# Kernel optimization log

Measured on AMD Instinct MI355X. Metric: run time of the kernel, lower is better.

The kernel has to match this reference:

```python
import jax, jax.numpy as jnp
import numpy as np

EPS = 1e-5
CLIP = 1.0

@jax.custom_vjp
def ste_sign(x):
    return jnp.sign(x)

def _ste_fwd(x):
    return jnp.sign(x), x

def _ste_bwd(x, g):
    return (g * (jnp.abs(x) <= CLIP).astype(g.dtype),)

ste_sign.defvjp(_ste_fwd, _ste_bwd)

def conv2d(x, w, stride, pad):
    return jax.lax.conv_general_dilated(
        x, w, window_strides=(stride, stride), padding=[(pad, pad), (pad, pad)],
        dimension_numbers=('NCHW', 'OIHW', 'NCHW'))

def bn(x, g, b, m, v):
    inv = g / jnp.sqrt(v + EPS)
    return x * inv[None, :, None, None] + (b - m * inv)[None, :, None, None]

def setup_inputs() -> dict:
    key = jax.random.key(0)
    ks = jax.random.split(key, 16)
    def rn(k, shape, scale=0.05):
        return jax.random.normal(k, shape, dtype=jnp.float32) * scale
    C = [64, 128, 128, 192, 192]
    d = {}
    d['x'] = jax.random.normal(ks[0], (128, 1, 128, 128), dtype=jnp.float32)
    d['conv1_w'] = rn(ks[1], (C[0], 1, 3, 3), 0.3)
    d['conv1_b'] = rn(ks[2], (C[0],))
    d['w2'] = rn(ks[3], (C[1], C[0], 3, 3), 0.3)
    d['w3'] = rn(ks[4], (C[2], C[1], 3, 3), 0.3)
    d['w4'] = rn(ks[5], (C[3], C[2], 3, 3), 0.3)
    d['w5'] = rn(ks[6], (C[4], C[3], 1, 1), 0.3)
    d['conv6_w'] = rn(ks[7], (12, C[4], 1, 1), 0.1)
    d['conv6_b'] = rn(ks[8], (12,))
    d['fc_w'] = rn(ks[9], (12, 12), 0.2)
    d['fc_b'] = rn(ks[10], (12,))
    for i, c in enumerate(C):
        kk = jax.random.split(jax.random.fold_in(key, 100 + i), 4)
        d[f'bn{i+1}_g'] = 1.0 + rn(kk[0], (c,), 0.1)
        d[f'bn{i+1}_b'] = rn(kk[1], (c,), 0.1)
        d[f'bn{i+1}_m'] = rn(kk[2], (c,), 0.1)
        d[f'bn{i+1}_v'] = 1.0 + jnp.abs(rn(kk[3], (c,), 0.1))
    return d

def reference(x, conv1_w, conv1_b, w2, w3, w4, w5, conv6_w, conv6_b, fc_w, fc_b,
              bn1_g, bn1_b, bn1_m, bn1_v, bn2_g, bn2_b, bn2_m, bn2_v,
              bn3_g, bn3_b, bn3_m, bn3_v, bn4_g, bn4_b, bn4_m, bn4_v,
              bn5_g, bn5_b, bn5_m, bn5_v):
    # conv1 (float) + BN + ReLU
    h = conv2d(x, conv1_w, 2, 1) + conv1_b[None, :, None, None]
    h = jax.nn.relu(bn(h, bn1_g, bn1_b, bn1_m, bn1_v))
    # binarized conv blocks: sign(activation) conv sign(weight)
    h = conv2d(ste_sign(h), ste_sign(w2), 1, 1)
    h = jax.nn.relu(bn(h, bn2_g, bn2_b, bn2_m, bn2_v))
    h = conv2d(ste_sign(h), ste_sign(w3), 2, 1)
    h = jax.nn.relu(bn(h, bn3_g, bn3_b, bn3_m, bn3_v))
    h = conv2d(ste_sign(h), ste_sign(w4), 1, 1)
    h = jax.nn.relu(bn(h, bn4_g, bn4_b, bn4_m, bn4_v))
    h = conv2d(ste_sign(h), ste_sign(w5), 1, 0)
    h = jax.nn.relu(bn(h, bn5_g, bn5_b, bn5_m, bn5_v))
    # 1x1 conv to classes, global average pool, FC, softmax
    h = conv2d(h, conv6_w, 1, 0) + conv6_b[None, :, None, None]
    h = jnp.mean(h, axis=(2, 3))  # [B, num_classes]
    logits = h @ fc_w.T + fc_b
    return jax.nn.softmax(logits, axis=1)
```

## Files before the change

kernel.cpp:

```cpp
#include <hip/hip_runtime.h>
#include <cstdint>

using u64 = unsigned long long;
using u32 = unsigned int;
typedef __attribute__((ext_vector_type(4))) int int4v;
typedef __attribute__((ext_vector_type(16))) int int16v;

struct PrepArgs {
  const float* bng[5]; const float* bnb[5]; const float* bnm[5]; const float* bnv[5];
  float* inv1; float* cc1; float* inv5; float* cc5;
  int* thr[3]; int* flp[3];
  const float* w[4];
  u64* wp[4]; u64* wz[4];
  u32* flags;
  const float* x; float* xpad;
  signed char* bf2x; signed char* bf3; signed char* bf4;
};

__device__ __forceinline__ void prep_all_body(const PrepArgs& a, int i) {
  if (i < 704) {
    const int off[6] = {0, 64, 192, 320, 512, 704};
    int l = 0;
    while (i >= off[l + 1]) ++l;
    int c = i - off[l];
    float iv = __fdiv_rn(a.bng[l][c], __fsqrt_rn(__fadd_rn(a.bnv[l][c], 1e-5f)));
    float cb = __fsub_rn(a.bnb[l][c], __fmul_rn(a.bnm[l][c], iv));
    if (l == 0) { a.inv1[c] = iv; a.cc1[c] = cb; }
    else if (l == 4) { a.inv5[c] = iv; a.cc5[c] = cb; }
    else {
      auto pred = [&](int v_) {
        return __fadd_rn(__fmul_rn((float)v_, iv), cb) > 0.f;
      };
      int Tx, fl;
      if (iv == 0.f) { Tx = pred(0) ? -100000 : 100000; fl = 0; }
      else if (iv > 0.f) {
        if (pred(-2048)) { Tx = -100000; fl = 0; }
        else if (!pred(2048)) { Tx = 100000; fl = 0; }
        else {
          int lo = -2048, hi = 2048;
          while (hi - lo > 1) { int md = (lo + hi) >> 1; if (pred(md)) hi = md; else lo = md; }
          Tx = hi; fl = 0;
        }
      } else {
        if (pred(2048)) { Tx = -100000; fl = -1; }
        else if (!pred(-2048)) { Tx = 100000; fl = -1; }
        else {
          int lo = -2048, hi = 2048;
          while (hi - lo > 1) { int md = (lo + hi) >> 1; if (pred(md)) lo = md; else hi = md; }
          Tx = lo ^ -1; fl = -1;
        }
      }
      a.thr[l - 1][c] = Tx; a.flp[l - 1][c] = fl;
    }
    return;
  }
  int j = i - 704;
  if (j >= 7488) return;
  const int poff[5] = {0, 1152, 3456, 6912, 7488};
  const int ICt[4] = {64, 128, 128, 192};
  const int Kt[4]  = {9, 9, 9, 1};
  const int Wt[4]  = {1, 2, 2, 3};
  int l = 0;
  while (j >= poff[l + 1]) ++l;
  int idx = j - poff[l];
  int W = Wt[l], K = Kt[l], IC = ICt[l];
  int wi = idx % W;
  int rest = idx / W;
  int t = rest % K;
  int oc = rest / K;
  u64 p = 0, z = 0;
  int icbase = wi * 64;
  int nb = IC - icbase; if (nb > 64) nb = 64;
  const float* w = a.w[l];
  for (int b = 0; b < nb; ++b) {
    float f = w[((size_t)oc * IC + (icbase + b)) * K + t];
    if (f > 0.f) p |= (1ull << b);
    else if (f == 0.f) z |= (1ull << b);
  }
  a.wp[l][idx] = p;
  a.wz[l][idx] = z;
  if (z) atomicOr(a.flags + l, 1u);
}

__device__ __forceinline__ void prep_bfrag32_body(const float* __restrict__ w,
                                                  signed char* __restrict__ bf, int idx) {
  if (idx >= 4 * 18 * 64) return;
  int lane = idx & 63;
  int rest = idx >> 6;
  int s = rest % 18;
  int t = rest / 18;
  int oc = t * 32 + (lane & 31);
  int kbase = s * 32 + (lane >> 5) * 16;
  signed char* dst = bf + (size_t)idx * 16;
#pragma unroll
  for (int i = 0; i < 16; ++i) {
    int k = kbase + i;
    int ch = k & 63, tap = k >> 6;
    float f = w[((size_t)oc * 64 + ch) * 9 + tap];
    dst[i] = (f > 0.f) ? 1 : ((f < 0.f) ? -1 : 0);
  }
}

template <int COUT>
__device__ __forceinline__ void prep_bfrag32b_body(const float* __restrict__ w,
                                                   signed char* __restrict__ bf, int idx) {
  constexpr int NT = COUT / 32;
  if (idx >= NT * 36 * 64) return;
  int lane = idx & 63;
  int rest = idx >> 6;
  int s = rest % 36;
  int t = rest / 36;
  int oc = t * 32 + (lane & 31);
  int kbase = s * 32 + (lane >> 5) * 16;
  signed char* dst = bf + (size_t)idx * 16;
#pragma unroll
  for (int i = 0; i < 16; ++i) {
    int k = kbase + i;
    int ch = k % 128, tap = k / 128;
    float f = w[((size_t)oc * 128 + ch) * 9 + tap];
    dst[i] = (f > 0.f) ? 1 : ((f < 0.f) ? -1 : 0);
  }
}

__global__ __launch_bounds__(256) void front(PrepArgs a) {
  int b = blockIdx.x, tid = threadIdx.x;
  if (b < 8192) {
    int idx = b * 256 + tid;
    int c = idx & 127, r = (idx >> 7) & 127, n = idx >> 14;
    a.xpad[((size_t)n * 130 + r + 1) * 136 + c + 1] = a.x[idx];
    return;
  }
  b -= 8192;
  if (b < 32) { prep_all_body(a, b * 256 + tid); return; }
  b -= 32;
  if (b < 18) { prep_bfrag32_body(a.w[0], a.bf2x, b * 256 + tid); return; }
  b -= 18;
  if (b < 36) { prep_bfrag32b_body<128>(a.w[1], a.bf3, b * 256 + tid); return; }
  b -= 36;
  if (b < 54) { prep_bfrag32b_body<192>(a.w[2], a.bf4, b * 256 + tid); return; }
}

__global__ __launch_bounds__(256) void conv1_bin(
    const float* __restrict__ xpad, const float* __restrict__ w1, const float* __restrict__ b1,
    const float* __restrict__ inv1, const float* __restrict__ cc1,
    u64* __restrict__ a1p) {
  int tid = threadIdx.x, lane = tid & 63;
  int rb = __builtin_amdgcn_readfirstlane(tid >> 6);
  int blk = blockIdx.x;
  int y = (blk % 16) * 4 + rb;
  int n = blk / 16;
  float W[9];
#pragma unroll
  for (int t = 0; t < 9; ++t) W[t] = w1[lane * 9 + t];
  float bias = b1[lane], iv = inv1[lane], cb = cc1[lane];
  const float* sb = xpad + ((size_t)n * 130 + 2 * y) * 136;
  float A[12], B[12], C[12];
  u64 rowm = 0;
  int xb = 0;

#define FLD(BUF, POFF)                                     \
  _Pragma("unroll") for (int _r = 0; _r < 3; ++_r)         \
  _Pragma("unroll") for (int _j = 0; _j < 4; ++_j)         \
    BUF[_r * 4 + _j] = sb[_r * 136 + (POFF) + _j];
#define FPX(XO, B0F, C0, B1F, C1, B2F, C2) {                          \
  float acc = 0.f;                                                    \
  _Pragma("unroll") for (int _r = 0; _r < 3; ++_r)                    \
    acc += B0F[_r * 4 + (C0)] * W[_r * 3 + 0]                         \
         + B1F[_r * 4 + (C1)] * W[_r * 3 + 1]                         \
         + B2F[_r * 4 + (C2)] * W[_r * 3 + 2];                        \
  float h = __fadd_rn(acc, bias);                                     \
  float bnv = __fadd_rn(__fmul_rn(h, iv), cb);                        \
  u64 _m = __ballot(bnv > 0.f);                                       \
  rowm = (lane == (XO)) ? _m : rowm; }
#define FSTEP(BA, BB, BC, POFF, XB)  \
  FLD(BC, (POFF) + 8);               \
  FPX((XB), BA, 0, BA, 1, BA, 2);    \
  FPX((XB) + 1, BA, 2, BA, 3, BB, 0);

  FLD(A, 0); FLD(B, 4);
  for (int g = 0; g < 10; ++g) {
    FSTEP(A, B, C, 0, xb);
    FSTEP(B, C, A, 4, xb + 2);
    FSTEP(C, A, B, 8, xb + 4);
    sb += 12; xb += 6;
  }
  FSTEP(A, B, C, 0, xb);
  FSTEP(B, C, A, 4, xb + 2);
  a1p[((size_t)n * 66 + (y + 1)) * 68 + lane + 1] = rowm;
#undef FLD
#undef FPX
#undef FSTEP
}

__global__ __launch_bounds__(256, 4) void bconv2_32(
    const u64* __restrict__ ain, const signed char* __restrict__ bf,
    const int* __restrict__ thr, const int* __restrict__ flp,
    u64* __restrict__ aout) {
  __shared__ int4v bs[2 * 18 * 64];
  int tid = threadIdx.x, lane = tid & 63;
  int wv = __builtin_amdgcn_readfirstlane(tid >> 6);
  int pos = blockIdx.x * 4 + wv;
  int xg = pos & 1;
  int y = (pos >> 1) & 63;
  int n = pos >> 7;
  int ln31 = lane & 31;
  int kg16 = (lane >> 5) * 16;
  int px = xg * 32 + ln31;

  const int4v* bfv = (const int4v*)bf;
  int4v breg[9];
#pragma unroll
  for (int i = 0; i < 9; ++i) breg[i] = bfv[tid + i * 256];

  const u64* abase = ain + ((size_t)n * 66 + y) * 68 + px;
  int4v af[18];
#pragma unroll
  for (int tap = 0; tap < 9; ++tap) {
    int dy = tap / 3, dx = tap % 3;
    u64 aw = abase[(size_t)dy * 68 + dx];
#pragma unroll
    for (int h = 0; h < 2; ++h) {
      u32 t16 = (u32)(aw >> (h * 32 + kg16)) & 0xFFFFu;
      int4v v;
      v.x = (int)((((t16      ) & 0xFu) * 0x00204081u) & 0x01010101u);
      v.y = (int)((((t16 >> 4 ) & 0xFu) * 0x00204081u) & 0x01010101u);
      v.z = (int)((((t16 >> 8 ) & 0xFu) * 0x00204081u) & 0x01010101u);
      v.w = (int)((((t16 >> 12) & 0xFu) * 0x00204081u) & 0x01010101u);
      af[tap * 2 + h] = v;
    }
  }

  int txv[4], flv[4];
#pragma unroll
  for (int t = 0; t < 4; ++t) { txv[t] = thr[t * 32 + ln31]; flv[t] = flp[t * 32 + ln31]; }

  u32* out32 = (u32*)aout;

#define C2_EPI(T, CREG) {                                             \
  int tx = txv[T], fl = flv[T];                                       \
  u32 oww = 0;                                                        \
  _Pragma("unroll") for (int r = 0; r < 16; ++r) {                    \
    int plo = (r & 3) + 8 * (r >> 2);                                 \
    u64 bal = __ballot((CREG[r] ^ fl) >= tx);                         \
    u32 wlo = (u32)bal, whi = (u32)(bal >> 32);                       \
    oww = (lane == plo) ? wlo : oww;                                  \
    oww = (lane == plo + 4) ? whi : oww;                              \
  }                                                                   \
  if (lane < 32) {                                                    \
    int xx = xg * 32 + lane;                                          \
    out32[(((size_t)n * 66 + (y + 1)) * 68 + (xx + 1)) * 4 + (T)] = oww; \
  } }

#pragma unroll
  for (int i = 0; i < 9; ++i) bs[tid + i * 256] = breg[i];
  __syncthreads();
#pragma unroll
  for (int i = 0; i < 9; ++i) breg[i] = bfv[2 * 18 * 64 + tid + i * 256];

#pragma unroll
  for (int t = 0; t < 2; ++t) {
    int16v c = {0, 0, 0, 0, 0, 0, 0, 0, 0, 0, 0, 0, 0, 0, 0, 0};
#pragma unroll
    for (int s = 0; s < 18; ++s) {
      int4v bb = bs[(t * 18 + s) * 64 + lane];
      c = __builtin_amdgcn_mfma_i32_32x32x32_i8(af[s], bb, c, 0, 0, 0);
    }
    C2_EPI(t, c)
  }

  __syncthreads();
#pragma unroll
  for (int i = 0; i < 9; ++i) bs[tid + i * 256] = breg[i];
  __syncthreads();
#pragma unroll
  for (int t = 2; t < 4; ++t) {
    int16v c = {0, 0, 0, 0, 0, 0, 0, 0, 0, 0, 0, 0, 0, 0, 0, 0};
#pragma unroll
    for (int s = 0; s < 18; ++s) {
      int4v bb = bs[((t - 2) * 18 + s) * 64 + lane];
      c = __builtin_amdgcn_mfma_i32_32x32x32_i8(af[s], bb, c, 0, 0, 0);
    }
    C2_EPI(t, c)
  }
#undef C2_EPI
}

template <int COUT, int STRIDE, int IN_HW, int OPAD>
__global__ __launch_bounds__(256) void bconv34_32(
    const u64* __restrict__ ain, const signed char* __restrict__ bf,
    const int* __restrict__ thr, const int* __restrict__ flp,
    u64* __restrict__ aout) {
  constexpr int IPW = IN_HW + 4;
  constexpr int NT = COUT / 32;
  constexpr int TW = 36 * 64;
  constexpr int OW32 = COUT / 32;
  __shared__ int4v bs[2][TW];
  int tid = threadIdx.x, lane = tid & 63;
  int wv = __builtin_amdgcn_readfirstlane(tid >> 6);
  int pos = blockIdx.x * 4 + wv;
  int y = pos & 31;
  int n = pos >> 5;
  int ln31 = lane & 31;
  int h = lane >> 5;

  const int4v* bfv = (const int4v*)bf;

  const u64* abase = ain + (((size_t)n * (IN_HW + 2) + (size_t)STRIDE * y) * IPW
                            + (size_t)STRIDE * ln31) * 2;
  int4v af[36];
#pragma unroll
  for (int tap = 0; tap < 9; ++tap) {
    int dy = tap / 3, dx = tap % 3;
    u64 w0 = abase[((size_t)dy * IPW + dx) * 2 + 0];
    u64 w1 = abase[((size_t)dy * IPW + dx) * 2 + 1];
#pragma unroll
    for (int q = 0; q < 4; ++q) {
      int m2 = 2 * q + h;
      u64 aw = (m2 & 4) ? w1 : w0;
      int sh = (m2 & 3) * 16;
      u32 t16 = (u32)(aw >> sh) & 0xFFFFu;
      int4v v;
      v.x = (int)((((t16      ) & 0xFu) * 0x00204081u) & 0x01010101u);
      v.y = (int)((((t16 >> 4 ) & 0xFu) * 0x00204081u) & 0x01010101u);
      v.z = (int)((((t16 >> 8 ) & 0xFu) * 0x00204081u) & 0x01010101u);
      v.w = (int)((((t16 >> 12) & 0xFu) * 0x00204081u) & 0x01010101u);
      af[tap * 4 + q] = v;
    }
  }

#pragma unroll
  for (int i = 0; i < 9; ++i) bs[0][tid + i * 256] = bfv[tid + i * 256];
  __syncthreads();

  u32* out32 = (u32*)aout;
  size_t px32;
  if (OPAD)
    px32 = (((size_t)n * 34 + (y + 1)) * 36 + (ln31 + 1)) * OW32;
  else
    px32 = (((size_t)n * 32 + y) * 32 + ln31) * OW32;

#pragma unroll 1
  for (int t = 0; t < NT; ++t) {
    if (t + 1 < NT) {
      const int4v* src = bfv + (size_t)(t + 1) * TW;
#pragma unroll
      for (int i = 0; i < 9; ++i) bs[(t + 1) & 1][tid + i * 256] = src[tid + i * 256];
    }
    int16v c = {0, 0, 0, 0, 0, 0, 0, 0, 0, 0, 0, 0, 0, 0, 0, 0};
#pragma unroll
    for (int s = 0; s < 36; ++s) {
      int4v bb = bs[t & 1][s * 64 + lane];
      c = __builtin_amdgcn_mfma_i32_32x32x32_i8(af[s], bb, c, 0, 0, 0);
    }
    int tx = thr[t * 32 + ln31];
    int fl = flp[t * 32 + ln31];
    u32 oww = 0;
#pragma unroll
    for (int r = 0; r < 16; ++r) {
      int plo = (r & 3) + 8 * (r >> 2);
      u64 bal = __ballot((c[r] ^ fl) >= tx);
      u32 wlo = (u32)bal, whi = (u32)(bal >> 32);
      oww = (lane == plo) ? wlo : oww;
      oww = (lane == plo + 4) ? whi : oww;
    }
    if (lane < 32) out32[px32 + t] = oww;
    __syncthreads();
  }
}

#define NCH5 8
__global__ __launch_bounds__(192) void bconv5_pool(
    const u64* __restrict__ ain, const u64* __restrict__ wp, const u64* __restrict__ wz,
    const u32* __restrict__ flag, const float* __restrict__ inv5, const float* __restrict__ cc5,
    float* __restrict__ partial) {
  int n = blockIdx.x / NCH5, ch = blockIdx.x % NCH5;
  int oc = threadIdx.x;
  u64 W0 = wp[oc * 3], W1 = wp[oc * 3 + 1], W2 = wp[oc * 3 + 2];
  bool anyz = (*flag != 0u);
  float iv = inv5[oc], cb = cc5[oc];
  const u64* sb = ain + ((size_t)n * 1024 + ch * 128) * 3;
  u64 A0, A1, A2, B0, B1, B2, C0, C1, C2;
  float acc = 0.f;
#define LD5(P, a0_, a1_, a2_) { a0_ = sb[(P) * 3]; a1_ = sb[(P) * 3 + 1]; a2_ = sb[(P) * 3 + 2]; }
#define PX5(a0_, a1_, a2_) {                                                   \
  int _pa = __popcll(a0_) + __popcll(a1_) + __popcll(a2_);                     \
  int _s = __popcll(a0_ & W0) + __popcll(a1_ & W1) + __popcll(a2_ & W2);       \
  int _val = 2 * _s - _pa;                                                     \
  if (anyz) _val += __popcll(a0_ & wz[oc * 3]) + __popcll(a1_ & wz[oc * 3 + 1])\
                  + __popcll(a2_ & wz[oc * 3 + 2]);                            \
  float _b = __fadd_rn(__fmul_rn((float)_val, iv), cb);                        \
  acc += fmaxf(_b, 0.f); }
  LD5(0, A0, A1, A2); LD5(1, B0, B1, B2);
  for (int g = 0; g < 42; ++g) {
    LD5(2, C0, C1, C2); PX5(A0, A1, A2);
    LD5(3, A0, A1, A2); PX5(B0, B1, B2);
    LD5(4, B0, B1, B2); PX5(C0, C1, C2);
    sb += 9;
  }
  PX5(A0, A1, A2); PX5(B0, B1, B2);
  partial[((size_t)n * NCH5 + ch) * 192 + oc] = acc;
#undef LD5
#undef PX5
}

__global__ __launch_bounds__(192) void head2(
    const float* __restrict__ partial,
    const float* __restrict__ w6, const float* __restrict__ b6,
    const float* __restrict__ fw, const float* __restrict__ fb,
    float* __restrict__ out) {
  __shared__ float pool_s[192];
  __shared__ float h6s[12];
  __shared__ float lgs[12];
  int n = blockIdx.x, t = threadIdx.x;
  float s = 0.f;
#pragma unroll
  for (int ch = 0; ch < NCH5; ++ch) s += partial[((size_t)n * NCH5 + ch) * 192 + t];
  pool_s[t] = s;
  __syncthreads();
  if (t < 12) {
    float a = 0.f;
    for (int c = 0; c < 192; ++c) a += pool_s[c] * w6[t * 192 + c];
    h6s[t] = b6[t] + a * (1.0f / 1024.0f);
  }
  __syncthreads();
  if (t < 12) {
    float s2 = fb[t];
    for (int k = 0; k < 12; ++k) s2 += h6s[k] * fw[t * 12 + k];
    lgs[t] = s2;
  }
  __syncthreads();
  if (t == 0) {
    float mx = -1e30f;
    for (int j = 0; j < 12; ++j) mx = fmaxf(mx, lgs[j]);
    float e[12], se = 0.f;
    for (int j = 0; j < 12; ++j) { e[j] = expf(lgs[j] - mx); se += e[j]; }
    for (int j = 0; j < 12; ++j) out[n * 12 + j] = e[j] / se;
  }
}

extern "C" void kernel_launch(void* const* d_in, const int* in_sizes, int n_in,
                              void* d_out, int out_size, void* d_ws, size_t ws_size,
                              hipStream_t stream) {
  const float* x   = (const float*)d_in[0];
  const float* w1  = (const float*)d_in[1];
  const float* b1  = (const float*)d_in[2];
  const float* w2  = (const float*)d_in[3];
  const float* w3  = (const float*)d_in[4];
  const float* w4  = (const float*)d_in[5];
  const float* w5  = (const float*)d_in[6];
  const float* w6  = (const float*)d_in[7];
  const float* b6  = (const float*)d_in[8];
  const float* fcw = (const float*)d_in[9];
  const float* fcb = (const float*)d_in[10];
  float* out = (float*)d_out;

  char* ws = (char*)d_ws;
  size_t off = 0;
  auto alloc = [&](size_t bytes) -> void* {
    void* p = ws + off;
    off += (bytes + 255) & ~(size_t)255;
    return p;
  };
  size_t xp_sz = (size_t)128 * 130 * 136 * 4;
  size_t a1_sz = (size_t)128 * 66 * 68 * 1 * 8;
  size_t a2_sz = (size_t)128 * 66 * 68 * 2 * 8;
  size_t a3_sz = (size_t)128 * 34 * 36 * 2 * 8;
  float* xpad = (float*)alloc(xp_sz);
  u64* a1p = (u64*)alloc(a1_sz);
  u64* a2p = (u64*)alloc(a2_sz);
  u64* a3p = (u64*)alloc(a3_sz);
  size_t zero_sz = xp_sz + a1_sz + a2_sz + a3_sz;
  u64* a4p = (u64*)alloc((size_t)128 * 32 * 32 * 3 * 8);
  float* partial = (float*)alloc((size_t)128 * NCH5 * 192 * 4);
  float* inv1 = (float*)alloc(64 * 4);
  float* cc1  = (float*)alloc(64 * 4);
  float* inv5 = (float*)alloc(192 * 4);
  float* cc5  = (float*)alloc(192 * 4);
  int* thr2 = (int*)alloc(128 * 4); int* flp2 = (int*)alloc(128 * 4);
  int* thr3 = (int*)alloc(128 * 4); int* flp3 = (int*)alloc(128 * 4);
  int* thr4 = (int*)alloc(192 * 4); int* flp4 = (int*)alloc(192 * 4);
  u64* wp2 = (u64*)alloc(128 * 9 * 1 * 8);
  u64* wz2 = (u64*)alloc(128 * 9 * 1 * 8);
  u64* wp3 = (u64*)alloc(128 * 9 * 2 * 8);
  u64* wz3 = (u64*)alloc(128 * 9 * 2 * 8);
  u64* wp4 = (u64*)alloc(192 * 9 * 2 * 8);
  u64* wz4 = (u64*)alloc(192 * 9 * 2 * 8);
  u64* wp5 = (u64*)alloc(192 * 1 * 3 * 8);
  u64* wz5 = (u64*)alloc(192 * 1 * 3 * 8);
  u32* flags = (u32*)alloc(4 * sizeof(u32));
  signed char* bf2x = (signed char*)alloc((size_t)4 * 18 * 64 * 16);
  signed char* bf3 = (signed char*)alloc((size_t)4 * 36 * 64 * 16);
  signed char* bf4 = (signed char*)alloc((size_t)6 * 36 * 64 * 16);
  (void)ws_size; (void)n_in; (void)in_sizes; (void)out_size;

  hipMemsetAsync(xpad, 0, zero_sz, stream);
  hipMemsetAsync(flags, 0, 4 * sizeof(u32), stream);

  PrepArgs pa;
  for (int l = 0; l < 5; ++l) {
    pa.bng[l] = (const float*)d_in[11 + 4 * l + 0];
    pa.bnb[l] = (const float*)d_in[11 + 4 * l + 1];
    pa.bnm[l] = (const float*)d_in[11 + 4 * l + 2];
    pa.bnv[l] = (const float*)d_in[11 + 4 * l + 3];
  }
  pa.inv1 = inv1; pa.cc1 = cc1; pa.inv5 = inv5; pa.cc5 = cc5;
  pa.thr[0] = thr2; pa.flp[0] = flp2;
  pa.thr[1] = thr3; pa.flp[1] = flp3;
  pa.thr[2] = thr4; pa.flp[2] = flp4;
  pa.w[0] = w2; pa.w[1] = w3; pa.w[2] = w4; pa.w[3] = w5;
  pa.wp[0] = wp2; pa.wp[1] = wp3; pa.wp[2] = wp4; pa.wp[3] = wp5;
  pa.wz[0] = wz2; pa.wz[1] = wz3; pa.wz[2] = wz4; pa.wz[3] = wz5;
  pa.flags = flags;
  pa.x = x; pa.xpad = xpad;
  pa.bf2x = bf2x; pa.bf3 = bf3; pa.bf4 = bf4;

  front<<<8192 + 32 + 18 + 36 + 54, 256, 0, stream>>>(pa);

  conv1_bin<<<128 * 16, 256, 0, stream>>>(xpad, w1, b1, inv1, cc1, a1p);

  bconv2_32<<<4096, 256, 0, stream>>>(a1p, bf2x, thr2, flp2, a2p);

  bconv34_32<128, 2, 64, 1><<<1024, 256, 0, stream>>>(
      a2p, bf3, thr3, flp3, a3p);

  bconv34_32<192, 1, 32, 0><<<1024, 256, 0, stream>>>(
      a3p, bf4, thr4, flp4, a4p);

  bconv5_pool<<<128 * NCH5, 192, 0, stream>>>(a4p, wp5, wz5, flags + 3, inv5, cc5, partial);

  head2<<<128, 192, 0, stream>>>(partial, w6, b6, fcw, fcb, out);
}
```

Before: 184.3 us.

## Store conv1 activations as int8 bytes instead of packed bitmasks

conv1 now writes one signed byte per channel and pixel into a padded int8 buffer, replacing the ballot-packed 64-bit masks. bconv2 loads its int8 A-fragments directly with vector loads instead of expanding bits via multiply/mask tricks. Guard borders of the new buffer are zeroed by extra blocks in the front kernel. This removes the ALU unpacking in bconv2 but increases the activation buffer size 64x, adding memory traffic in both conv1 (byte stores) and bconv2 loads.

New measurement: 185.5 us. Within noise of the previous version (+0.7%).

```diff
diff --git a/kernel.cpp b/kernel.cpp
--- a/kernel.cpp
+++ b/kernel.cpp
@@ -15,6 +15,7 @@
   u32* flags;
   const float* x; float* xpad;
   signed char* bf2x; signed char* bf3; signed char* bf4;
+  signed char* a1i8;
 };
 
 __device__ __forceinline__ void prep_all_body(const PrepArgs& a, int i) {
@@ -122,6 +123,18 @@
   }
 }
 
+__device__ __forceinline__ void guard_zero_body(signed char* __restrict__ a1i8, int idx) {
+  if (idx >= 128 * 392) return;
+  int n = idx / 392, g = idx % 392;
+  int r, c;
+  if (g < 68) { r = 0; c = g; }
+  else if (g < 136) { r = 65; c = g - 68; }
+  else { int q = g - 136; r = 1 + (q >> 2); int cc = q & 3; c = (cc == 0) ? 0 : 64 + cc; }
+  int4v z = {0, 0, 0, 0};
+  int4v* dst = (int4v*)(a1i8 + ((size_t)(n * 66 + r) * 68 + c) * 64);
+  dst[0] = z; dst[1] = z; dst[2] = z; dst[3] = z;
+}
+
 __global__ __launch_bounds__(256) void front(PrepArgs a) {
   int b = blockIdx.x, tid = threadIdx.x;
   if (b < 8192) {
@@ -138,12 +151,14 @@
   if (b < 36) { prep_bfrag32b_body<128>(a.w[1], a.bf3, b * 256 + tid); return; }
   b -= 36;
   if (b < 54) { prep_bfrag32b_body<192>(a.w[2], a.bf4, b * 256 + tid); return; }
+  b -= 54;
+  if (b < 196) { guard_zero_body(a.a1i8, b * 256 + tid); return; }
 }
 
 __global__ __launch_bounds__(256) void conv1_bin(
     const float* __restrict__ xpad, const float* __restrict__ w1, const float* __restrict__ b1,
     const float* __restrict__ inv1, const float* __restrict__ cc1,
-    u64* __restrict__ a1p) {
+    signed char* __restrict__ a1i8) {
   int tid = threadIdx.x, lane = tid & 63;
   int rb = __builtin_amdgcn_readfirstlane(tid >> 6);
   int blk = blockIdx.x;
@@ -154,8 +169,8 @@
   for (int t = 0; t < 9; ++t) W[t] = w1[lane * 9 + t];
   float bias = b1[lane], iv = inv1[lane], cb = cc1[lane];
   const float* sb = xpad + ((size_t)n * 130 + 2 * y) * 136;
+  signed char* a1row = a1i8 + (((size_t)n * 66 + (y + 1)) * 68 + 1) * 64;
   float A[12], B[12], C[12];
-  u64 rowm = 0;
   int xb = 0;
 
 #define FLD(BUF, POFF)                                     \
@@ -170,8 +185,7 @@
          + B2F[_r * 4 + (C2)] * W[_r * 3 + 2];                        \
   float h = __fadd_rn(acc, bias);                                     \
   float bnv = __fadd_rn(__fmul_rn(h, iv), cb);                        \
-  u64 _m = __ballot(bnv > 0.f);                                       \
-  rowm = (lane == (XO)) ? _m : rowm; }
+  a1row[(size_t)(XO) * 64 + lane] = (signed char)(bnv > 0.f ? 1 : 0); }
 #define FSTEP(BA, BB, BC, POFF, XB)  \
   FLD(BC, (POFF) + 8);               \
   FPX((XB), BA, 0, BA, 1, BA, 2);    \
@@ -186,14 +200,13 @@
   }
   FSTEP(A, B, C, 0, xb);
   FSTEP(B, C, A, 4, xb + 2);
-  a1p[((size_t)n * 66 + (y + 1)) * 68 + lane + 1] = rowm;
 #undef FLD
 #undef FPX
 #undef FSTEP
 }
 
 __global__ __launch_bounds__(256, 4) void bconv2_32(
-    const u64* __restrict__ ain, const signed char* __restrict__ bf,
+    const signed char* __restrict__ a1i8, const signed char* __restrict__ bf,
     const int* __restrict__ thr, const int* __restrict__ flp,
     u64* __restrict__ aout) {
   __shared__ int4v bs[2 * 18 * 64];
@@ -212,22 +225,14 @@
 #pragma unroll
   for (int i = 0; i < 9; ++i) breg[i] = bfv[tid + i * 256];
 
-  const u64* abase = ain + ((size_t)n * 66 + y) * 68 + px;
+  const signed char* a1b = a1i8 + (((size_t)n * 66 + y) * 68 + px) * 64 + kg16;
   int4v af[18];
 #pragma unroll
   for (int tap = 0; tap < 9; ++tap) {
     int dy = tap / 3, dx = tap % 3;
-    u64 aw = abase[(size_t)dy * 68 + dx];
-#pragma unroll
-    for (int h = 0; h < 2; ++h) {
-      u32 t16 = (u32)(aw >> (h * 32 + kg16)) & 0xFFFFu;
-      int4v v;
-      v.x = (int)((((t16      ) & 0xFu) * 0x00204081u) & 0x01010101u);
-      v.y = (int)((((t16 >> 4 ) & 0xFu) * 0x00204081u) & 0x01010101u);
-      v.z = (int)((((t16 >> 8 ) & 0xFu) * 0x00204081u) & 0x01010101u);
-      v.w = (int)((((t16 >> 12) & 0xFu) * 0x00204081u) & 0x01010101u);
-      af[tap * 2 + h] = v;
-    }
+    const signed char* p = a1b + ((size_t)dy * 68 + dx) * 64;
+    af[tap * 2 + 0] = *(const int4v*)(p);
+    af[tap * 2 + 1] = *(const int4v*)(p + 32);
   }
 
   int txv[4], flv[4];
@@ -462,14 +467,13 @@
     return p;
   };
   size_t xp_sz = (size_t)128 * 130 * 136 * 4;
-  size_t a1_sz = (size_t)128 * 66 * 68 * 1 * 8;
   size_t a2_sz = (size_t)128 * 66 * 68 * 2 * 8;
   size_t a3_sz = (size_t)128 * 34 * 36 * 2 * 8;
   float* xpad = (float*)alloc(xp_sz);
-  u64* a1p = (u64*)alloc(a1_sz);
   u64* a2p = (u64*)alloc(a2_sz);
   u64* a3p = (u64*)alloc(a3_sz);
-  size_t zero_sz = xp_sz + a1_sz + a2_sz + a3_sz;
+  size_t zero_sz = xp_sz + a2_sz + a3_sz;
+  signed char* a1i8 = (signed char*)alloc((size_t)128 * 66 * 68 * 64);
   u64* a4p = (u64*)alloc((size_t)128 * 32 * 32 * 3 * 8);
   float* partial = (float*)alloc((size_t)128 * NCH5 * 192 * 4);
   float* inv1 = (float*)alloc(64 * 4);
@@ -513,12 +517,13 @@
   pa.flags = flags;
   pa.x = x; pa.xpad = xpad;
   pa.bf2x = bf2x; pa.bf3 = bf3; pa.bf4 = bf4;
-
-  front<<<8192 + 32 + 18 + 36 + 54, 256, 0, stream>>>(pa);
-
-  conv1_bin<<<128 * 16, 256, 0, stream>>>(xpad, w1, b1, inv1, cc1, a1p);
-
-  bconv2_32<<<4096, 256, 0, stream>>>(a1p, bf2x, thr2, flp2, a2p);
+  pa.a1i8 = a1i8;
+
+  front<<<8192 + 32 + 18 + 36 + 54 + 196, 256, 0, stream>>>(pa);
+
+  conv1_bin<<<128 * 16, 256, 0, stream>>>(xpad, w1, b1, inv1, cc1, a1i8);
+
+  bconv2_32<<<4096, 256, 0, stream>>>(a1i8, bf2x, thr2, flp2, a2p);
 
   bconv34_32<128, 2, 64, 1><<<1024, 256, 0, stream>>>(
       a2p, bf3, thr3, flp3, a3p);
```
